# Optimization experiments

Hardware: AMD Instinct MI355X
Metric: run time of the kernel (lower is better)

## Reference

```python
import jax, jax.numpy as jnp
import numpy as np

B, C, CI, H, W = 4, 128, 64, 96, 96  # batch, in_channels, inter_channels, spatial
SS = 2                                # sub_sample_factor (maxpool on phi and g)
BN_EPS = 1e-5


def conv1x1(x, w, b):
    # x: [B,C,H,W], w: [O,C], b: [O]
    return jnp.einsum('bchw,oc->bohw', x, w) + b[None, :, None, None]


def maxpool2(x):
    # 2x2 max pool, stride 2. x: [B,C,H,W]
    b, c, h, w = x.shape
    return x.reshape(b, c, h // 2, 2, w // 2, 2).max(axis=(3, 5))


def setup_inputs() -> dict:
    key = jax.random.key(0)
    ks = jax.random.split(key, 12)
    s_in = 1.0 / np.sqrt(C)
    s_ci = 1.0 / np.sqrt(CI)
    return {
        'x':        jax.random.normal(ks[0], (B, C, H, W), jnp.float32),
        'g_w':      jax.random.normal(ks[1], (CI, C), jnp.float32) * s_in,
        'g_b':      jax.random.normal(ks[2], (CI,), jnp.float32) * 0.01,
        'theta_w':  jax.random.normal(ks[3], (CI, C), jnp.float32) * s_in,
        'theta_b':  jax.random.normal(ks[4], (CI,), jnp.float32) * 0.01,
        'phi_w':    jax.random.normal(ks[5], (CI, C), jnp.float32) * s_in,
        'phi_b':    jax.random.normal(ks[6], (CI,), jnp.float32) * 0.01,
        'W_w':      jax.random.normal(ks[7], (C, CI), jnp.float32) * s_ci,
        'W_b':      jax.random.normal(ks[8], (C,), jnp.float32) * 0.01,
        'bn_gamma': jax.random.normal(ks[9], (C,), jnp.float32) * 0.1 + 1.0,
        'bn_beta':  jax.random.normal(ks[10], (C,), jnp.float32) * 0.1,
        'bn_mean':  jax.random.normal(ks[11], (C,), jnp.float32) * 0.1,
        'bn_var':   jax.random.uniform(jax.random.fold_in(key, 99), (C,), jnp.float32, 0.5, 1.5),
    }


def reference(x, g_w, g_b, theta_w, theta_b, phi_w, phi_b, W_w, W_b,
              bn_gamma, bn_beta, bn_mean, bn_var):
    b = x.shape[0]
    # g: conv1x1 -> maxpool(2) -> [B, N_kv, CI]
    g_x = maxpool2(conv1x1(x, g_w, g_b)).reshape(b, CI, -1).transpose(0, 2, 1)
    # theta: conv1x1 -> [B, N_q, CI]
    theta_x = conv1x1(x, theta_w, theta_b).reshape(b, CI, -1).transpose(0, 2, 1)
    # phi: conv1x1 -> maxpool(2) -> [B, CI, N_kv]
    phi_x = maxpool2(conv1x1(x, phi_w, phi_b)).reshape(b, CI, -1)
    # full affinity [B, N_q, N_kv], softmax over keys (embedded_gaussian)
    f = jnp.einsum('bqc,bck->bqk', theta_x, phi_x)
    attn = jax.nn.softmax(f, axis=-1)
    y = jnp.einsum('bqk,bkc->bqc', attn, g_x)            # [B, N_q, CI]
    y = y.transpose(0, 2, 1).reshape(b, CI, H, W)
    # W: conv1x1 (CI -> C) + BatchNorm (inference form) + residual
    W_y = conv1x1(y, W_w, W_b)
    inv = bn_gamma * jax.lax.rsqrt(bn_var + BN_EPS)
    W_y = W_y * inv[None, :, None, None] + (bn_beta - bn_mean * inv)[None, :, None, None]
    return W_y + x
```

## Files before the change

### kernel.cpp

```cpp
#include <hip/hip_runtime.h>
#include <hip/hip_bf16.h>

#define NB 4
#define NC 128
#define NH 96
#define NQ 9216
#define NKV 2304

typedef __bf16 bf8 __attribute__((ext_vector_type(8)));
typedef float f4 __attribute__((ext_vector_type(4)));
typedef unsigned short u16t;
typedef unsigned int u32t;
typedef u32t u32x4 __attribute__((ext_vector_type(4)));
typedef u16t u16x4v __attribute__((ext_vector_type(4)));

static __device__ __forceinline__ u16t f2bf(float f){
  u32t u = __builtin_bit_cast(u32t, f);
  u = (u + 0x7fffu + ((u >> 16) & 1u)) >> 16;
  return (u16t)u;
}
static __device__ __forceinline__ float bf2f(u16t h){
  return __builtin_bit_cast(float, ((u32t)h) << 16);
}

static __device__ __forceinline__ f4 mfma16(bf8 a, bf8 b, f4 c){
  return __builtin_amdgcn_mfma_f32_16x16x32_bf16(a, b, c, 0, 0, 0);
}

#define GLDS16(gp, lp) __builtin_amdgcn_global_load_lds( \
    (const u32t*)(gp), (u32t*)(lp), 16, 0, 0)

__global__ __launch_bounds__(256) void prep_weights(
    const float* __restrict__ g_w, const float* __restrict__ theta_w,
    const float* __restrict__ phi_w, const float* __restrict__ W_w,
    const float* __restrict__ W_b, const float* __restrict__ bn_gamma,
    const float* __restrict__ bn_beta, const float* __restrict__ bn_mean,
    const float* __restrict__ bn_var,
    u16t* __restrict__ wt_theta, u16t* __restrict__ wt_phi,
    u16t* __restrict__ wt_g, u16t* __restrict__ wt_W,
    float* __restrict__ alpha, float* __restrict__ beta2)
{
  int i = blockIdx.x * 256 + threadIdx.x;
  wt_theta[i] = f2bf(theta_w[i]);
  wt_phi[i]   = f2bf(phi_w[i]);
  wt_g[i]     = f2bf(g_w[i]);
  wt_W[i]     = f2bf(W_w[i]);
  if (blockIdx.x == 0 && threadIdx.x < 128){
    int t = threadIdx.x;
    float inv = bn_gamma[t] * rsqrtf(bn_var[t] + 1e-5f);
    alpha[t] = inv;
    beta2[t] = W_b[t]*inv + bn_beta[t] - bn_mean[t]*inv;
  }
}

__global__ __launch_bounds__(256) void conv3_pool(
    const float* __restrict__ x,
    const u16t* __restrict__ wt_theta, const u16t* __restrict__ wt_phi,
    const u16t* __restrict__ wt_g,
    const float* __restrict__ theta_b, const float* __restrict__ phi_b,
    const float* __restrict__ g_b,
    u16t* __restrict__ theta, u16t* __restrict__ phi, u16t* __restrict__ g_t)
{
  __shared__ __align__(16) u16t xt[64][136];
  const int blk = blockIdx.x;
  const int batch = blk / 144;
  const int t144 = blk % 144;
  const int ph = t144 / 3;
  const int pw0 = (t144 % 3) * 16;
  const int t = threadIdx.x;
  const float* xb = x + (size_t)batch * NC * NQ;

  #pragma unroll
  for (int i = 0; i < 8; ++i){
    int slot = i*256 + t;
    int c = slot >> 4;
    int quad = slot & 15;
    int row = quad >> 3, col4 = (quad & 7)*4;
    int q = (ph*2 + row)*NH + pw0*2 + col4;
    float4 v = *(const float4*)&xb[(size_t)c*NQ + q];
    int pl = row*32 + col4;
    u32t lo, hi;
    asm("v_cvt_pk_bf16_f32 %0, %1, %2" : "=v"(lo) : "v"(v.x), "v"(v.y));
    asm("v_cvt_pk_bf16_f32 %0, %1, %2" : "=v"(hi) : "v"(v.z), "v"(v.w));
    xt[pl+0][c] = (u16t)lo;
    xt[pl+1][c] = (u16t)(lo >> 16);
    xt[pl+2][c] = (u16t)hi;
    xt[pl+3][c] = (u16t)(hi >> 16);
  }
  __syncthreads();

  const int w = t >> 6, l = t & 63, lm = l & 15, lg = l >> 4;
  auto PL = [](int pxi){
    return (((pxi>>1)&1) << 5) + 8*(pxi>>4) + 2*((pxi>>2)&3) + (pxi&1);
  };
  auto QROW = [&](int pxi){
    return (ph*2 + ((pxi>>1)&1))*NH + (pw0 + 4*(pxi>>4) + ((pxi>>2)&3))*2 + (pxi&1);
  };
  bf8 a[4];
  #pragma unroll
  for (int k = 0; k < 4; ++k)
    a[k] = *(const bf8*)&xt[PL(w*16 + lm)][k*32 + lg*8];

  const int kvbase = ph*48 + pw0;
  const int kv = kvbase + 4*w + lg;

  f4 Dth[4];
  #pragma unroll
  for (int s = 0; s < 4; ++s){
    float bv = theta_b[s*16 + lm];
    f4 D = {bv, bv, bv, bv};
    #pragma unroll
    for (int k = 0; k < 4; ++k){
      bf8 b = *(const bf8*)&wt_theta[(s*16 + lm)*128 + k*32 + lg*8];
      D = mfma16(a[k], b, D);
    }
    Dth[s] = D;
  }
  {
    u16t* pp = phi + (size_t)batch * NKV * 64;
    #pragma unroll
    for (int s = 0; s < 4; ++s){
      float bv = phi_b[s*16 + lm];
      f4 D = {bv, bv, bv, bv};
      #pragma unroll
      for (int k = 0; k < 4; ++k){
        bf8 b = *(const bf8*)&wt_phi[(s*16 + lm)*128 + k*32 + lg*8];
        D = mfma16(a[k], b, D);
      }
      float mx = fmaxf(fmaxf(D[0], D[1]), fmaxf(D[2], D[3]));
      pp[(size_t)kv*64 + s*16 + lm] = f2bf(mx);
    }
  }
  float gmx[4];
  #pragma unroll
  for (int s = 0; s < 4; ++s){
    float bv = g_b[s*16 + lm];
    f4 D = {bv, bv, bv, bv};
    #pragma unroll
    for (int k = 0; k < 4; ++k){
      bf8 b = *(const bf8*)&wt_g[(s*16 + lm)*128 + k*32 + lg*8];
      D = mfma16(a[k], b, D);
    }
    gmx[s] = fmaxf(fmaxf(D[0], D[1]), fmaxf(D[2], D[3]));
  }

  __syncthreads();
  u16t* tl = &xt[0][0];
  u16t* gl = &xt[0][0] + 4608;
  #pragma unroll
  for (int s = 0; s < 4; ++s){
    #pragma unroll
    for (int r = 0; r < 4; ++r)
      tl[(w*16 + lg*4 + r)*72 + s*16 + lm] = f2bf(Dth[s][r]);
    gl[(s*16 + lm)*20 + 4*w + lg] = f2bf(gmx[s]);
  }
  __syncthreads();
  {
    u16t* th = theta + (size_t)batch * NQ * 64;
    #pragma unroll
    for (int p = 0; p < 2; ++p){
      int slot = t + 256*p;
      int row = slot >> 3, piece = slot & 7;
      int q = QROW(row);
      *(bf8*)&th[(size_t)q*64 + piece*8] = *(const bf8*)&tl[row*72 + piece*8];
    }
  }
  {
    u16t* gt = g_t + (size_t)batch * 64 * NKV;
    int c = t >> 2, L = t & 3;
    int T = (kvbase >> 4) & 3;
    int kvg = kvbase & ~63;
    u16x4v v;
    #pragma unroll
    for (int u = 0; u < 4; ++u) v[u] = gl[c*20 + L*4 + u];
    *(u16x4v*)&gt[(size_t)c*NKV + kvg + (T>>1)*32 + ((T&1)<<2) + L*8] = v;
  }
}


__global__ __launch_bounds__(256) void attn_partial(
    const u16t* __restrict__ theta, const u16t* __restrict__ phi,
    const u16t* __restrict__ g_t,
    u16t* __restrict__ yp_ws, float* __restrict__ sums_ws)
{
  __shared__ __align__(16) char SM[32768];

  const int bid = blockIdx.x;
  const int blkL = (bid & 7)*96 + (bid >> 3);
  const int batch = blkL / 192;
  const int rem = blkL % 192;
  const int qb = (rem >> 1) * 96;
  const int khb = rem & 1;
  const int t = threadIdx.x;
  const int w = t >> 6, l = t & 63, lm = l & 15, lg = l >> 4;
  const int qw = w >> 1, khw = w & 1;

  const u16t* th = theta + ((size_t)batch*NQ + qb)*64;
  bf8 a[3][2];
  #pragma unroll
  for (int mr = 0; mr < 3; ++mr){
    a[mr][0] = *(const bf8*)&th[(qw*48 + mr*16 + lm)*64 + lg*8];
    a[mr][1] = *(const bf8*)&th[(qw*48 + mr*16 + lm)*64 + 32 + lg*8];
  }
  asm volatile("s_waitcnt vmcnt(0)" ::: "memory");

  const char* phc = (const char*)(phi + (size_t)batch*NKV*64);
  const char* gtc = (const char*)(g_t + (size_t)batch*64*NKV);

  auto STAGE = [&](int kt_s, int bufc){
    #pragma unroll
    for (int j = 0; j < 4; ++j){
      int u = w*4 + j;
      int khu = u >> 3, isg = (u >> 2) & 1, sub = u & 3;
      int kb = khb*1152 + khu*576 + kt_s*32;
      char* dst;
      const char* src;
      if (!isg){
        int row = sub*8 + (l >> 3);
        int swz = ((l & 7) ^ (l >> 3)) << 4;
        dst = SM + (khu*2 + bufc)*4096 + sub*1024 + l*16;
        src = phc + (size_t)(kb + row)*128 + swz;
      } else {
        int row = sub*16 + (l >> 2);
        int swz = (((l & 3) ^ ((l >> 2) & 3)) << 4);
        dst = SM + 16384 + (khu*2 + bufc)*4096 + sub*1024 + l*16;
        src = gtc + (size_t)row*(NKV*2) + (size_t)kb*2 + swz;
      }
      GLDS16(src, dst);
    }
  };

  f4 Y[3][4];
  #pragma unroll
  for (int mr = 0; mr < 3; ++mr)
    #pragma unroll
    for (int s = 0; s < 4; ++s)
      Y[mr][s] = f4{0.f, 0.f, 0.f, 0.f};
  float lsum[3] = {0.f, 0.f, 0.f};

  STAGE(0, 0);

  for (int kt = 0; kt < 18; ++kt){
    const int buf = kt & 1;
    __builtin_amdgcn_s_barrier();
    asm volatile("" ::: "memory");
    if (kt < 17){
      STAGE(kt + 1, buf ^ 1);
      asm volatile("s_waitcnt vmcnt(4)" ::: "memory");
    } else {
      asm volatile("s_waitcnt vmcnt(0)" ::: "memory");
    }
    __builtin_amdgcn_s_barrier();
    asm volatile("" ::: "memory");
    __builtin_amdgcn_sched_barrier(0);

    const char* pb = SM + (khw*2 + buf)*4096;
    const char* gb = SM + 16384 + (khw*2 + buf)*4096;
    const int m7 = lm & 7;

    bf8 bp[2][2];
    #pragma unroll
    for (int tt = 0; tt < 2; ++tt){
      int rb = (tt*16 + lm)*128;
      bp[tt][0] = *(const bf8*)(pb + rb + ((lg ^ m7) << 4));
      bp[tt][1] = *(const bf8*)(pb + rb + (((4 + lg) ^ m7) << 4));
    }
    bf8 bg[4];
    #pragma unroll
    for (int s = 0; s < 4; ++s){
      int rb = (s*16 + lm)*64;
      bg[s] = *(const bf8*)(gb + rb + ((lg ^ (lm & 3)) << 4));
    }

    #pragma unroll
    for (int mr = 0; mr < 3; ++mr){
      f4 S[2];
      #pragma unroll
      for (int tt = 0; tt < 2; ++tt){
        f4 z = {0.f, 0.f, 0.f, 0.f};
        z = mfma16(bp[tt][0], a[mr][0], z);
        S[tt] = mfma16(bp[tt][1], a[mr][1], z);
      }
      u32t wq[4];
      #pragma unroll
      for (int tt = 0; tt < 2; ++tt){
        float p0, p1, p2, p3;
        float a0 = fmaf(S[tt][0], 1.44269504f, -43.2808512f);
        float a1 = fmaf(S[tt][1], 1.44269504f, -43.2808512f);
        float a2 = fmaf(S[tt][2], 1.44269504f, -43.2808512f);
        float a3 = fmaf(S[tt][3], 1.44269504f, -43.2808512f);
        asm("v_exp_f32 %0, %1" : "=v"(p0) : "v"(a0));
        asm("v_exp_f32 %0, %1" : "=v"(p1) : "v"(a1));
        asm("v_exp_f32 %0, %1" : "=v"(p2) : "v"(a2));
        asm("v_exp_f32 %0, %1" : "=v"(p3) : "v"(a3));
        lsum[mr] += (p0 + p1) + (p2 + p3);
        asm("v_cvt_pk_bf16_f32 %0, %1, %2" : "=v"(wq[tt*2])   : "v"(p0), "v"(p1));
        asm("v_cvt_pk_bf16_f32 %0, %1, %2" : "=v"(wq[tt*2+1]) : "v"(p2), "v"(p3));
      }
      bf8 pa = __builtin_bit_cast(bf8, u32x4{wq[0], wq[1], wq[2], wq[3]});
      #pragma unroll
      for (int s = 0; s < 4; ++s)
        Y[mr][s] = mfma16(pa, bg[s], Y[mr][s]);
    }
  }

  float sv[3];
  #pragma unroll
  for (int mr = 0; mr < 3; ++mr){
    float s0 = lsum[mr];
    s0 += __shfl_xor(s0, 16);
    s0 += __shfl_xor(s0, 32);
    sv[mr] = s0;
  }

  __syncthreads();
  float (*ypL)[68] = (float (*)[68])SM;
  if (khw == 0){
    #pragma unroll
    for (int mr = 0; mr < 3; ++mr){
      #pragma unroll
      for (int s = 0; s < 4; ++s)
        #pragma unroll
        for (int r = 0; r < 4; ++r)
          ypL[qw*48 + mr*16 + lg*4 + r][s*16 + lm] = Y[mr][s][r];
      if (lg == 0)
        ypL[qw*48 + mr*16 + lm][64] = sv[mr];
    }
  }
  __syncthreads();
  if (khw == 1){
    #pragma unroll
    for (int mr = 0; mr < 3; ++mr){
      #pragma unroll
      for (int s = 0; s < 4; ++s)
        #pragma unroll
        for (int r = 0; r < 4; ++r)
          ypL[qw*48 + mr*16 + lg*4 + r][s*16 + lm] += Y[mr][s][r];
      if (lg == 0)
        ypL[qw*48 + mr*16 + lm][64] += sv[mr];
    }
  }
  __syncthreads();

  u16t* ypg = yp_ws + (size_t)blkL * (96*64);
  float* sg  = sums_ws + (size_t)blkL * 96;
  #pragma unroll
  for (int i = 0; i < 6; ++i){
    int idx = t + 256*i;
    int q = idx >> 4, c4 = (idx & 15)*4;
    u16x4v v;
    #pragma unroll
    for (int j = 0; j < 4; ++j) v[j] = f2bf(ypL[q][c4 + j]);
    *(u16x4v*)&ypg[q*64 + c4] = v;
  }
  if (t < 96) sg[t] = ypL[t][64];
}

__global__ __launch_bounds__(256) void combine_out(
    const u16t* __restrict__ yp_ws, const float* __restrict__ sums_ws,
    const u16t* __restrict__ wt_W,
    const float* __restrict__ alpha, const float* __restrict__ beta2,
    const float* __restrict__ x, float* __restrict__ out)
{
  __shared__ __align__(16) u16t yl[96][72];
  __shared__ __align__(16) float ol[96][131];
  const int bid = blockIdx.x;
  const int blk = (bid & 7)*48 + (bid >> 3);
  const int batch = blk / 96;
  const int qg = blk % 96;
  const int qb = qg * 96;
  const int t = threadIdx.x;
  const int w = t >> 6, l = t & 63, lm = l & 15, lg = l >> 4;

  const u16t* pA = yp_ws + ((size_t)batch*192 + qg*2) * (96*64);
  const u16t* pB = pA + 96*64;
  const float* sA = sums_ws + ((size_t)batch*192 + qg*2) * 96;
  const float* sB = sA + 96;

  #pragma unroll
  for (int i = 0; i < 6; ++i){
    int idx = t + 256*i;
    int q = idx >> 4, c4 = (idx & 15)*4;
    float inv = 1.0f / (sA[q] + sB[q]);
    u16x4v a4 = *(const u16x4v*)&pA[q*64 + c4];
    u16x4v b4 = *(const u16x4v*)&pB[q*64 + c4];
    u16x4v v;
    #pragma unroll
    for (int j = 0; j < 4; ++j)
      v[j] = f2bf((bf2f(a4[j]) + bf2f(b4[j])) * inv);
    *(u16x4v*)&yl[q][c4] = v;
  }
  __syncthreads();

  #pragma unroll
  for (int i = 0; i < 12; ++i){
    int tau = w + 4*i;
    int qt = tau >> 3, ct = tau & 7;
    bf8 ya0 = *(const bf8*)&yl[qt*16 + lm][lg*8];
    bf8 ya1 = *(const bf8*)&yl[qt*16 + lm][32 + lg*8];
    const u16t* wr = wt_W + (ct*16 + lm)*64;
    bf8 b0 = *(const bf8*)&wr[lg*8];
    bf8 b1 = *(const bf8*)&wr[lg*8 + 32];
    f4 z = {0.f, 0.f, 0.f, 0.f};
    z = mfma16(ya0, b0, z);
    z = mfma16(ya1, b1, z);
    #pragma unroll
    for (int r = 0; r < 4; ++r)
      ol[qt*16 + lg*4 + r][ct*16 + lm] = z[r];
  }
  __syncthreads();

  const float* xb = x + (size_t)batch*NC*NQ + qb;
  float* ob = out + (size_t)batch*NC*NQ + qb;
  #pragma unroll
  for (int i = 0; i < 12; ++i){
    int idx = t + 256*i;
    int c = idx / 24, qv = idx % 24;
    float4 xv = *(const float4*)&xb[(size_t)c*NQ + qv*4];
    float al = alpha[c], be = beta2[c];
    float4 ov;
    ov.x = ol[qv*4 + 0][c]*al + be + xv.x;
    ov.y = ol[qv*4 + 1][c]*al + be + xv.y;
    ov.z = ol[qv*4 + 2][c]*al + be + xv.z;
    ov.w = ol[qv*4 + 3][c]*al + be + xv.w;
    *(float4*)&ob[(size_t)c*NQ + qv*4] = ov;
  }
}

extern "C" void kernel_launch(void* const* d_in, const int* in_sizes, int n_in,
                              void* d_out, int out_size, void* d_ws, size_t ws_size,
                              hipStream_t stream)
{
  const float* x       = (const float*)d_in[0];
  const float* g_w     = (const float*)d_in[1];
  const float* g_b     = (const float*)d_in[2];
  const float* theta_w = (const float*)d_in[3];
  const float* theta_b = (const float*)d_in[4];
  const float* phi_w   = (const float*)d_in[5];
  const float* phi_b   = (const float*)d_in[6];
  const float* W_w     = (const float*)d_in[7];
  const float* W_b     = (const float*)d_in[8];
  const float* bn_g    = (const float*)d_in[9];
  const float* bn_b    = (const float*)d_in[10];
  const float* bn_m    = (const float*)d_in[11];
  const float* bn_v    = (const float*)d_in[12];
  float* out = (float*)d_out;

  char* ws = (char*)d_ws;
  size_t off = 0;
  u16t* theta = (u16t*)(ws + off); off += (size_t)NB*NQ*64*2;
  u16t* phi   = (u16t*)(ws + off); off += (size_t)NB*NKV*64*2;
  u16t* g_t   = (u16t*)(ws + off); off += (size_t)NB*64*NKV*2;
  u16t* wt_theta = (u16t*)(ws + off); off += 64*128*2;
  u16t* wt_phi   = (u16t*)(ws + off); off += 64*128*2;
  u16t* wt_g     = (u16t*)(ws + off); off += 64*128*2;
  u16t* wt_W     = (u16t*)(ws + off); off += 128*64*2;
  float* alpha = (float*)(ws + off); off += 128*4;
  float* beta2 = (float*)(ws + off); off += 128*4;
  u16t* yp_ws  = (u16t*)(ws + off); off += (size_t)768*96*64*2;
  float* sums_ws = (float*)(ws + off); off += (size_t)768*96*4;
  if (off > ws_size) return;

  prep_weights<<<32, 256, 0, stream>>>(g_w, theta_w, phi_w, W_w, W_b,
                                       bn_g, bn_b, bn_m, bn_v,
                                       wt_theta, wt_phi, wt_g, wt_W, alpha, beta2);
  conv3_pool<<<576, 256, 0, stream>>>(x, wt_theta, wt_phi, wt_g,
                                      theta_b, phi_b, g_b, theta, phi, g_t);
  attn_partial<<<768, 256, 0, stream>>>(theta, phi, g_t, yp_ws, sums_ws);
  combine_out<<<384, 256, 0, stream>>>(yp_ws, sums_ws, wt_W, alpha, beta2, x, out);
}
```

Baseline: 75.99 us.

## Fuse attention partials with output projection into one 512-thread kernel

Merges the split-KV attention kernel and the combine/projection kernel into one kernel of 512 threads per block. Each block now covers all keys for its 96 queries with four key-splitting waves, reduces the partials in shared memory, and applies the W projection, BN and residual directly. This removes the bf16 partial workspace round trip and one kernel launch. In exchange the grid halves to 384 blocks and LDS use rises to 64KB per block, which may lower occupancy and latency hiding.

```diff
diff --git a/kernel.cpp b/kernel.cpp
--- a/kernel.cpp
+++ b/kernel.cpp
@@ -18,9 +18,6 @@
   u32t u = __builtin_bit_cast(u32t, f);
   u = (u + 0x7fffu + ((u >> 16) & 1u)) >> 16;
   return (u16t)u;
-}
-static __device__ __forceinline__ float bf2f(u16t h){
-  return __builtin_bit_cast(float, ((u32t)h) << 16);
 }
 
 static __device__ __forceinline__ f4 mfma16(bf8 a, bf8 b, f4 c){
@@ -178,22 +175,21 @@
 }
 
 
-__global__ __launch_bounds__(256) void attn_partial(
+__global__ __launch_bounds__(512) void attn_fused(
     const u16t* __restrict__ theta, const u16t* __restrict__ phi,
-    const u16t* __restrict__ g_t,
-    u16t* __restrict__ yp_ws, float* __restrict__ sums_ws)
+    const u16t* __restrict__ g_t, const u16t* __restrict__ wt_W,
+    const float* __restrict__ alpha, const float* __restrict__ beta2,
+    const float* __restrict__ x, float* __restrict__ out)
 {
-  __shared__ __align__(16) char SM[32768];
+  __shared__ __align__(16) char SM[65536];
 
   const int bid = blockIdx.x;
-  const int blkL = (bid & 7)*96 + (bid >> 3);
-  const int batch = blkL / 192;
-  const int rem = blkL % 192;
-  const int qb = (rem >> 1) * 96;
-  const int khb = rem & 1;
+  const int blk = (bid & 7)*48 + (bid >> 3);
+  const int batch = blk / 96;
+  const int qb = (blk % 96) * 96;
   const int t = threadIdx.x;
   const int w = t >> 6, l = t & 63, lm = l & 15, lg = l >> 4;
-  const int qw = w >> 1, khw = w & 1;
+  const int qw = w >> 2, khw = w & 3;
 
   const u16t* th = theta + ((size_t)batch*NQ + qb)*64;
   bf8 a[3][2];
@@ -212,7 +208,7 @@
     for (int j = 0; j < 4; ++j){
       int u = w*4 + j;
       int khu = u >> 3, isg = (u >> 2) & 1, sub = u & 3;
-      int kb = khb*1152 + khu*576 + kt_s*32;
+      int kb = khu*576 + kt_s*32;
       char* dst;
       const char* src;
       if (!isg){
@@ -223,7 +219,7 @@
       } else {
         int row = sub*16 + (l >> 2);
         int swz = (((l & 3) ^ ((l >> 2) & 3)) << 4);
-        dst = SM + 16384 + (khu*2 + bufc)*4096 + sub*1024 + l*16;
+        dst = SM + 32768 + (khu*2 + bufc)*4096 + sub*1024 + l*16;
         src = gtc + (size_t)row*(NKV*2) + (size_t)kb*2 + swz;
       }
       GLDS16(src, dst);
@@ -255,7 +251,7 @@
     __builtin_amdgcn_sched_barrier(0);
 
     const char* pb = SM + (khw*2 + buf)*4096;
-    const char* gb = SM + 16384 + (khw*2 + buf)*4096;
+    const char* gb = SM + 32768 + (khw*2 + buf)*4096;
     const int m7 = lm & 7;
 
     bf8 bp[2][2];
@@ -314,90 +310,58 @@
   }
 
   __syncthreads();
-  float (*ypL)[68] = (float (*)[68])SM;
-  if (khw == 0){
+  float (*ypA)[66] = (float (*)[66])SM;
+  float (*ypB)[66] = (float (*)[66])(SM + 25344);
+  float (*myp)[66] = (khw < 2) ? ypA : ypB;
+  if ((khw & 1) == 0){
     #pragma unroll
     for (int mr = 0; mr < 3; ++mr){
       #pragma unroll
       for (int s = 0; s < 4; ++s)
         #pragma unroll
         for (int r = 0; r < 4; ++r)
-          ypL[qw*48 + mr*16 + lg*4 + r][s*16 + lm] = Y[mr][s][r];
+          myp[qw*48 + mr*16 + lg*4 + r][s*16 + lm] = Y[mr][s][r];
       if (lg == 0)
-        ypL[qw*48 + mr*16 + lm][64] = sv[mr];
-    }
-  }
-  __syncthreads();
-  if (khw == 1){
+        myp[qw*48 + mr*16 + lm][64] = sv[mr];
+    }
+  }
+  __syncthreads();
+  if ((khw & 1) == 1){
     #pragma unroll
     for (int mr = 0; mr < 3; ++mr){
       #pragma unroll
       for (int s = 0; s < 4; ++s)
         #pragma unroll
         for (int r = 0; r < 4; ++r)
-          ypL[qw*48 + mr*16 + lg*4 + r][s*16 + lm] += Y[mr][s][r];
+          myp[qw*48 + mr*16 + lg*4 + r][s*16 + lm] += Y[mr][s][r];
       if (lg == 0)
-        ypL[qw*48 + mr*16 + lm][64] += sv[mr];
-    }
-  }
-  __syncthreads();
-
-  u16t* ypg = yp_ws + (size_t)blkL * (96*64);
-  float* sg  = sums_ws + (size_t)blkL * 96;
+        myp[qw*48 + mr*16 + lm][64] += sv[mr];
+    }
+  }
+  __syncthreads();
+
+  u16t* yl = (u16t*)(SM + 50688);
   #pragma unroll
   for (int i = 0; i < 6; ++i){
-    int idx = t + 256*i;
-    int q = idx >> 4, c4 = (idx & 15)*4;
-    u16x4v v;
-    #pragma unroll
-    for (int j = 0; j < 4; ++j) v[j] = f2bf(ypL[q][c4 + j]);
-    *(u16x4v*)&ypg[q*64 + c4] = v;
-  }
-  if (t < 96) sg[t] = ypL[t][64];
-}
-
-__global__ __launch_bounds__(256) void combine_out(
-    const u16t* __restrict__ yp_ws, const float* __restrict__ sums_ws,
-    const u16t* __restrict__ wt_W,
-    const float* __restrict__ alpha, const float* __restrict__ beta2,
-    const float* __restrict__ x, float* __restrict__ out)
-{
-  __shared__ __align__(16) u16t yl[96][72];
-  __shared__ __align__(16) float ol[96][131];
-  const int bid = blockIdx.x;
-  const int blk = (bid & 7)*48 + (bid >> 3);
-  const int batch = blk / 96;
-  const int qg = blk % 96;
-  const int qb = qg * 96;
-  const int t = threadIdx.x;
-  const int w = t >> 6, l = t & 63, lm = l & 15, lg = l >> 4;
-
-  const u16t* pA = yp_ws + ((size_t)batch*192 + qg*2) * (96*64);
-  const u16t* pB = pA + 96*64;
-  const float* sA = sums_ws + ((size_t)batch*192 + qg*2) * 96;
-  const float* sB = sA + 96;
-
+    int p = t + 512*i;
+    int q = p >> 5, cp = p & 31;
+    float tot = ypA[q][64] + ypB[q][64];
+    float inv = 1.0f / tot;
+    float v0 = (ypA[q][cp*2]     + ypB[q][cp*2])     * inv;
+    float v1 = (ypA[q][cp*2 + 1] + ypB[q][cp*2 + 1]) * inv;
+    u32t pk;
+    asm("v_cvt_pk_bf16_f32 %0, %1, %2" : "=v"(pk) : "v"(v0), "v"(v1));
+    *(u32t*)&yl[q*72 + cp*2] = pk;
+  }
+  __syncthreads();
+
+  float (*ol)[131] = (float (*)[131])SM;
   #pragma unroll
   for (int i = 0; i < 6; ++i){
-    int idx = t + 256*i;
-    int q = idx >> 4, c4 = (idx & 15)*4;
-    float inv = 1.0f / (sA[q] + sB[q]);
-    u16x4v a4 = *(const u16x4v*)&pA[q*64 + c4];
-    u16x4v b4 = *(const u16x4v*)&pB[q*64 + c4];
-    u16x4v v;
-    #pragma unroll
-    for (int j = 0; j < 4; ++j)
-      v[j] = f2bf((bf2f(a4[j]) + bf2f(b4[j])) * inv);
-    *(u16x4v*)&yl[q][c4] = v;
-  }
-  __syncthreads();
-
-  #pragma unroll
-  for (int i = 0; i < 12; ++i){
-    int tau = w + 4*i;
+    int tau = w + 8*i;
     int qt = tau >> 3, ct = tau & 7;
-    bf8 ya0 = *(const bf8*)&yl[qt*16 + lm][lg*8];
-    bf8 ya1 = *(const bf8*)&yl[qt*16 + lm][32 + lg*8];
+    bf8 ya0 = *(const bf8*)&yl[(qt*16 + lm)*72 + lg*8];
+    bf8 ya1 = *(const bf8*)&yl[(qt*16 + lm)*72 + 32 + lg*8];
     const u16t* wr = wt_W + (ct*16 + lm)*64;
     bf8 b0 = *(const bf8*)&wr[lg*8];
     bf8 b1 = *(const bf8*)&wr[lg*8 + 32];
@@ -413,8 +377,8 @@
   const float* xb = x + (size_t)batch*NC*NQ + qb;
   float* ob = out + (size_t)batch*NC*NQ + qb;
   #pragma unroll
-  for (int i = 0; i < 12; ++i){
-    int idx = t + 256*i;
+  for (int i = 0; i < 6; ++i){
+    int idx = t + 512*i;
     int c = idx / 24, qv = idx % 24;
     float4 xv = *(const float4*)&xb[(size_t)c*NQ + qv*4];
     float al = alpha[c], be = beta2[c];
@@ -457,8 +421,6 @@
   u16t* wt_W     = (u16t*)(ws + off); off += 128*64*2;
   float* alpha = (float*)(ws + off); off += 128*4;
   float* beta2 = (float*)(ws + off); off += 128*4;
-  u16t* yp_ws  = (u16t*)(ws + off); off += (size_t)768*96*64*2;
-  float* sums_ws = (float*)(ws + off); off += (size_t)768*96*4;
   if (off > ws_size) return;
 
   prep_weights<<<32, 256, 0, stream>>>(g_w, theta_w, phi_w, W_w, W_b,
@@ -466,6 +428,5 @@
                                        wt_theta, wt_phi, wt_g, wt_W, alpha, beta2);
   conv3_pool<<<576, 256, 0, stream>>>(x, wt_theta, wt_phi, wt_g,
                                       theta_b, phi_b, g_b, theta, phi, g_t);
-  attn_partial<<<768, 256, 0, stream>>>(theta, phi, g_t, yp_ws, sums_ws);
-  combine_out<<<384, 256, 0, stream>>>(yp_ws, sums_ws, wt_W, alpha, beta2, x, out);
-}
+  attn_fused<<<384, 512, 0, stream>>>(theta, phi, g_t, wt_W, alpha, beta2, x, out);
+}
```

Result: slower. 80.66 us (+6.1%).

## Enlarge attention tiles to 288 queries per block across six waves

Applied to the files above, without the earlier changes.

Each attention block now covers 288 queries with six waves and a full key-half per block, staging 64 keys per step in place of 32. Every wave runs the whole key range, so the cross-wave partial reduction in LDS goes away. Each staged phi/g tile is now shared by six waves instead of two. The partial-output workspace is re-indexed per batch and key-half, and combine_out reads it with the new layout. The trade-off is 76 KB of LDS and 256 large blocks, which means roughly one block of six waves per CU and less latency hiding.

```diff
diff --git a/kernel.cpp b/kernel.cpp
--- a/kernel.cpp
+++ b/kernel.cpp
@@ -178,29 +178,29 @@
 }
 
 
-__global__ __launch_bounds__(256) void attn_partial(
+__global__ __launch_bounds__(384) void attn_partial(
     const u16t* __restrict__ theta, const u16t* __restrict__ phi,
     const u16t* __restrict__ g_t,
     u16t* __restrict__ yp_ws, float* __restrict__ sums_ws)
 {
-  __shared__ __align__(16) char SM[32768];
+  __shared__ __align__(16) char SM[76032];
 
   const int bid = blockIdx.x;
-  const int blkL = (bid & 7)*96 + (bid >> 3);
-  const int batch = blkL / 192;
-  const int rem = blkL % 192;
-  const int qb = (rem >> 1) * 96;
+  const int blkL = (bid & 7)*32 + (bid >> 3);
+  const int batch = blkL >> 6;
+  const int rem = blkL & 63;
+  const int qt = rem >> 1;
   const int khb = rem & 1;
+  const int qb = qt * 288;
   const int t = threadIdx.x;
   const int w = t >> 6, l = t & 63, lm = l & 15, lg = l >> 4;
-  const int qw = w >> 1, khw = w & 1;
 
   const u16t* th = theta + ((size_t)batch*NQ + qb)*64;
   bf8 a[3][2];
   #pragma unroll
   for (int mr = 0; mr < 3; ++mr){
-    a[mr][0] = *(const bf8*)&th[(qw*48 + mr*16 + lm)*64 + lg*8];
-    a[mr][1] = *(const bf8*)&th[(qw*48 + mr*16 + lm)*64 + 32 + lg*8];
+    a[mr][0] = *(const bf8*)&th[(w*48 + mr*16 + lm)*64 + lg*8];
+    a[mr][1] = *(const bf8*)&th[(w*48 + mr*16 + lm)*64 + 32 + lg*8];
   }
   asm volatile("s_waitcnt vmcnt(0)" ::: "memory");
 
@@ -209,22 +209,21 @@
 
   auto STAGE = [&](int kt_s, int bufc){
     #pragma unroll
-    for (int j = 0; j < 4; ++j){
-      int u = w*4 + j;
-      int khu = u >> 3, isg = (u >> 2) & 1, sub = u & 3;
-      int kb = khb*1152 + khu*576 + kt_s*32;
+    for (int j = 0; j < 3; ++j){
+      int u = w*3 + j;
+      int ur = (u < 16) ? u : (u - 16);
+      int isg = ur >> 3, sub = ur & 7;
+      int kb = khb*1152 + kt_s*64;
+      int row8 = sub*8 + (l >> 3);
+      int swz = ((l & 7) ^ (l >> 3)) << 4;
       char* dst;
       const char* src;
       if (!isg){
-        int row = sub*8 + (l >> 3);
-        int swz = ((l & 7) ^ (l >> 3)) << 4;
-        dst = SM + (khu*2 + bufc)*4096 + sub*1024 + l*16;
-        src = phc + (size_t)(kb + row)*128 + swz;
+        dst = SM + bufc*8192 + sub*1024 + l*16;
+        src = phc + (size_t)(kb + row8)*128 + swz;
       } else {
-        int row = sub*16 + (l >> 2);
-        int swz = (((l & 3) ^ ((l >> 2) & 3)) << 4);
-        dst = SM + 16384 + (khu*2 + bufc)*4096 + sub*1024 + l*16;
-        src = gtc + (size_t)row*(NKV*2) + (size_t)kb*2 + swz;
+        dst = SM + 16384 + bufc*8192 + sub*1024 + l*16;
+        src = gtc + (size_t)row8*(NKV*2) + (size_t)kb*2 + swz;
       }
       GLDS16(src, dst);
     }
@@ -246,7 +245,7 @@
     asm volatile("" ::: "memory");
     if (kt < 17){
       STAGE(kt + 1, buf ^ 1);
-      asm volatile("s_waitcnt vmcnt(4)" ::: "memory");
+      asm volatile("s_waitcnt vmcnt(3)" ::: "memory");
     } else {
       asm volatile("s_waitcnt vmcnt(0)" ::: "memory");
     }
@@ -254,36 +253,37 @@
     asm volatile("" ::: "memory");
     __builtin_amdgcn_sched_barrier(0);
 
-    const char* pb = SM + (khw*2 + buf)*4096;
-    const char* gb = SM + 16384 + (khw*2 + buf)*4096;
+    const char* pb = SM + buf*8192;
+    const char* gb = SM + 16384 + buf*8192;
     const int m7 = lm & 7;
 
-    bf8 bp[2][2];
-    #pragma unroll
-    for (int tt = 0; tt < 2; ++tt){
+    bf8 bp[4][2];
+    #pragma unroll
+    for (int tt = 0; tt < 4; ++tt){
       int rb = (tt*16 + lm)*128;
       bp[tt][0] = *(const bf8*)(pb + rb + ((lg ^ m7) << 4));
       bp[tt][1] = *(const bf8*)(pb + rb + (((4 + lg) ^ m7) << 4));
     }
-    bf8 bg[4];
+    bf8 bg[4][2];
     #pragma unroll
     for (int s = 0; s < 4; ++s){
-      int rb = (s*16 + lm)*64;
-      bg[s] = *(const bf8*)(gb + rb + ((lg ^ (lm & 3)) << 4));
+      int rb = (s*16 + lm)*128;
+      bg[s][0] = *(const bf8*)(gb + rb + ((lg ^ m7) << 4));
+      bg[s][1] = *(const bf8*)(gb + rb + (((4 + lg) ^ m7) << 4));
     }
 
     #pragma unroll
     for (int mr = 0; mr < 3; ++mr){
-      f4 S[2];
+      f4 S[4];
       #pragma unroll
-      for (int tt = 0; tt < 2; ++tt){
+      for (int tt = 0; tt < 4; ++tt){
         f4 z = {0.f, 0.f, 0.f, 0.f};
         z = mfma16(bp[tt][0], a[mr][0], z);
         S[tt] = mfma16(bp[tt][1], a[mr][1], z);
       }
-      u32t wq[4];
+      u32t wq[8];
       #pragma unroll
-      for (int tt = 0; tt < 2; ++tt){
+      for (int tt = 0; tt < 4; ++tt){
         float p0, p1, p2, p3;
         float a0 = fmaf(S[tt][0], 1.44269504f, -43.2808512f);
         float a1 = fmaf(S[tt][1], 1.44269504f, -43.2808512f);
@@ -297,10 +297,13 @@
         asm("v_cvt_pk_bf16_f32 %0, %1, %2" : "=v"(wq[tt*2])   : "v"(p0), "v"(p1));
         asm("v_cvt_pk_bf16_f32 %0, %1, %2" : "=v"(wq[tt*2+1]) : "v"(p2), "v"(p3));
       }
-      bf8 pa = __builtin_bit_cast(bf8, u32x4{wq[0], wq[1], wq[2], wq[3]});
+      bf8 pa0 = __builtin_bit_cast(bf8, u32x4{wq[0], wq[1], wq[2], wq[3]});
+      bf8 pa1 = __builtin_bit_cast(bf8, u32x4{wq[4], wq[5], wq[6], wq[7]});
       #pragma unroll
-      for (int s = 0; s < 4; ++s)
-        Y[mr][s] = mfma16(pa, bg[s], Y[mr][s]);
+      for (int s = 0; s < 4; ++s){
+        Y[mr][s] = mfma16(pa0, bg[s][0], Y[mr][s]);
+        Y[mr][s] = mfma16(pa1, bg[s][1], Y[mr][s]);
+      }
     }
   }
 
@@ -314,46 +317,31 @@
   }
 
   __syncthreads();
-  float (*ypL)[68] = (float (*)[68])SM;
-  if (khw == 0){
-    #pragma unroll
-    for (int mr = 0; mr < 3; ++mr){
+  float (*ypL)[66] = (float (*)[66])SM;
+  #pragma unroll
+  for (int mr = 0; mr < 3; ++mr){
+    #pragma unroll
+    for (int s = 0; s < 4; ++s)
       #pragma unroll
-      for (int s = 0; s < 4; ++s)
-        #pragma unroll
-        for (int r = 0; r < 4; ++r)
-          ypL[qw*48 + mr*16 + lg*4 + r][s*16 + lm] = Y[mr][s][r];
-      if (lg == 0)
-        ypL[qw*48 + mr*16 + lm][64] = sv[mr];
-    }
-  }
-  __syncthreads();
-  if (khw == 1){
-    #pragma unroll
-    for (int mr = 0; mr < 3; ++mr){
-      #pragma unroll
-      for (int s = 0; s < 4; ++s)
-        #pragma unroll
-        for (int r = 0; r < 4; ++r)
-          ypL[qw*48 + mr*16 + lg*4 + r][s*16 + lm] += Y[mr][s][r];
-      if (lg == 0)
-        ypL[qw*48 + mr*16 + lm][64] += sv[mr];
-    }
-  }
-  __syncthreads();
-
-  u16t* ypg = yp_ws + (size_t)blkL * (96*64);
-  float* sg  = sums_ws + (size_t)blkL * 96;
-  #pragma unroll
-  for (int i = 0; i < 6; ++i){
-    int idx = t + 256*i;
+      for (int r = 0; r < 4; ++r)
+        ypL[w*48 + mr*16 + lg*4 + r][s*16 + lm] = Y[mr][s][r];
+    if (lg == 0)
+      ypL[w*48 + mr*16 + lm][64] = sv[mr];
+  }
+  __syncthreads();
+
+  u16t* ypg = yp_ws + ((size_t)(batch*2 + khb)*NQ + qb) * 64;
+  float* sg  = sums_ws + (size_t)(batch*2 + khb)*NQ + qb;
+  #pragma unroll
+  for (int i = 0; i < 12; ++i){
+    int idx = t + 384*i;
     int q = idx >> 4, c4 = (idx & 15)*4;
     u16x4v v;
     #pragma unroll
     for (int j = 0; j < 4; ++j) v[j] = f2bf(ypL[q][c4 + j]);
     *(u16x4v*)&ypg[q*64 + c4] = v;
   }
-  if (t < 96) sg[t] = ypL[t][64];
+  if (t < 288) sg[t] = ypL[t][64];
 }
 
 __global__ __launch_bounds__(256) void combine_out(
@@ -372,10 +360,10 @@
   const int t = threadIdx.x;
   const int w = t >> 6, l = t & 63, lm = l & 15, lg = l >> 4;
 
-  const u16t* pA = yp_ws + ((size_t)batch*192 + qg*2) * (96*64);
-  const u16t* pB = pA + 96*64;
-  const float* sA = sums_ws + ((size_t)batch*192 + qg*2) * 96;
-  const float* sB = sA + 96;
+  const u16t* pA = yp_ws + ((size_t)(batch*2 + 0)*NQ + qb)*64;
+  const u16t* pB = yp_ws + ((size_t)(batch*2 + 1)*NQ + qb)*64;
+  const float* sA = sums_ws + (size_t)(batch*2 + 0)*NQ + qb;
+  const float* sB = sums_ws + (size_t)(batch*2 + 1)*NQ + qb;
 
   #pragma unroll
   for (int i = 0; i < 6; ++i){
@@ -457,8 +445,8 @@
   u16t* wt_W     = (u16t*)(ws + off); off += 128*64*2;
   float* alpha = (float*)(ws + off); off += 128*4;
   float* beta2 = (float*)(ws + off); off += 128*4;
-  u16t* yp_ws  = (u16t*)(ws + off); off += (size_t)768*96*64*2;
-  float* sums_ws = (float*)(ws + off); off += (size_t)768*96*4;
+  u16t* yp_ws  = (u16t*)(ws + off); off += (size_t)8*NQ*64*2;
+  float* sums_ws = (float*)(ws + off); off += (size_t)8*NQ*4;
   if (off > ws_size) return;
 
   prep_weights<<<32, 256, 0, stream>>>(g_w, theta_w, phi_w, W_w, W_b,
@@ -466,6 +454,6 @@
                                        wt_theta, wt_phi, wt_g, wt_W, alpha, beta2);
   conv3_pool<<<576, 256, 0, stream>>>(x, wt_theta, wt_phi, wt_g,
                                       theta_b, phi_b, g_b, theta, phi, g_t);
-  attn_partial<<<768, 256, 0, stream>>>(theta, phi, g_t, yp_ws, sums_ws);
+  attn_partial<<<256, 384, 0, stream>>>(theta, phi, g_t, yp_ws, sums_ws);
   combine_out<<<384, 256, 0, stream>>>(yp_ws, sums_ws, wt_W, alpha, beta2, x, out);
 }
```

Result: slower. 77.81 us (+2.4%).
